# Performance work log

Measured on AMD Instinct MI355X. Metric: run time of the kernel, lower is better.

Reference implementation:

```python
import jax, jax.numpy as jnp
import numpy as np

N = 100_000      # nodes
E = 1_600_000    # edges (before self-loops)
IN = 128         # in_channels
HID = 32         # hidden_channels
HEADS = 2        # attention heads
OUT = 64         # out_channels
NEG_SLOPE = 0.2  # PyG GATConv leaky-relu slope


def setup_inputs() -> dict:
    key = jax.random.key(0)
    ks = jax.random.split(key, 16)
    HC = HID * HEADS

    def glorot(k, shape, fan_in):
        return jax.random.normal(k, shape, jnp.float32) / np.sqrt(fan_in)

    return {
        "x": jax.random.normal(ks[0], (N, IN), jnp.float32),
        "edge_index": jax.random.randint(ks[1], (2, E), 0, N, jnp.int64),
        # layer 1: IN -> HID per head, concat
        "W1": glorot(ks[2], (IN, HC), IN),
        "as1": glorot(ks[3], (HEADS, HID), HID),
        "ad1": glorot(ks[4], (HEADS, HID), HID),
        "b1": jnp.zeros((HC,), jnp.float32),
        # layer 2: HC -> HID per head, concat
        "W2": glorot(ks[5], (HC, HC), HC),
        "as2": glorot(ks[6], (HEADS, HID), HID),
        "ad2": glorot(ks[7], (HEADS, HID), HID),
        "b2": jnp.zeros((HC,), jnp.float32),
        # layer 3: HC -> OUT, 1 head, no concat
        "W3": glorot(ks[8], (HC, OUT), HC),
        "as3": glorot(ks[9], (1, OUT), OUT),
        "ad3": glorot(ks[10], (1, OUT), OUT),
        "b3": jnp.zeros((OUT,), jnp.float32),
    }


def gat_conv(x, src, dst, W, a_src, a_dst, b, heads, out_ch, concat, n):
    # per-head linear transform: [n, heads, out_ch]
    h = (x @ W).reshape(n, heads, out_ch)
    # per-node attention logits: [n, heads]
    al_src = jnp.einsum('nhc,hc->nh', h, a_src)
    al_dst = jnp.einsum('nhc,hc->nh', h, a_dst)
    # raw edge scores with leaky relu: [e, heads]
    e = al_src[src] + al_dst[dst]
    e = jnp.where(e >= 0, e, NEG_SLOPE * e)
    # segment softmax over incoming edges of each dst node
    m = jax.ops.segment_max(e, dst, num_segments=n)          # [n, heads]
    ee = jnp.exp(e - m[dst])
    denom = jax.ops.segment_sum(ee, dst, num_segments=n)     # [n, heads]
    alpha = ee / denom[dst]
    # weighted scatter-add of source features
    out = jax.ops.segment_sum(h[src] * alpha[..., None], dst, num_segments=n)
    if concat:
        out = out.reshape(n, heads * out_ch)
    else:
        out = out.mean(axis=1)
    return out + b


def reference(x, edge_index, W1, as1, ad1, b1, W2, as2, ad2, b2, W3, as3, ad3, b3):
    # PyG GATConv adds self-loops by default
    loop = jnp.arange(N, dtype=edge_index.dtype)
    src = jnp.concatenate([edge_index[0], loop])
    dst = jnp.concatenate([edge_index[1], loop])

    h = gat_conv(x, src, dst, W1, as1, ad1, b1, HEADS, HID, True, N)
    h = jax.nn.relu(h)
    h = gat_conv(h, src, dst, W2, as2, ad2, b2, HEADS, HID, True, N)
    h = jax.nn.relu(h)
    out = gat_conv(h, src, dst, W3, as3, ad3, b3, 1, OUT, False, N)
    return out
```

## Files before the change

### kernel.cpp

```cpp
#include <hip/hip_runtime.h>
#include <hip/hip_fp16.h>

#define IN_CH   128
#define HC      64
#define NEG_SLOPE 0.2f

#define BSH   9
#define NPB   512
#define EPB   8192
#define DBIN  64

typedef __attribute__((ext_vector_type(8))) _Float16 f16x8;
typedef __attribute__((ext_vector_type(4))) float    f32x4;

__global__ __launch_bounds__(256) void scan1_k(const int* __restrict__ deg, int* __restrict__ tmp,
                                               int* __restrict__ bsum, int n) {
    __shared__ int s[256];
    int tid = threadIdx.x;
    int i = blockIdx.x * 256 + tid;
    int v = (i < n) ? deg[i] : 0;
    s[tid] = v; __syncthreads();
    for (int o = 1; o < 256; o <<= 1) {
        int t = (tid >= o) ? s[tid - o] : 0;
        __syncthreads();
        s[tid] += t;
        __syncthreads();
    }
    if (i < n) tmp[i] = s[tid] - v;
    if (tid == 255) bsum[blockIdx.x] = s[255];
}

__global__ __launch_bounds__(512) void scan2_k(int* __restrict__ bsum, int nb) {
    __shared__ int s[512];
    int tid = threadIdx.x;
    int v = (tid < nb) ? bsum[tid] : 0;
    s[tid] = v; __syncthreads();
    for (int o = 1; o < 512; o <<= 1) {
        int t = (tid >= o) ? s[tid - o] : 0;
        __syncthreads();
        s[tid] += t;
        __syncthreads();
    }
    if (tid < nb) bsum[tid] = s[tid] - v;
}

__global__ __launch_bounds__(256) void combine_k(const int* __restrict__ tmp, const int* __restrict__ bsum,
                                                 int* __restrict__ base, int n) {
    int i = blockIdx.x * 256 + threadIdx.x;
    if (i < n) base[i] = tmp[i] + bsum[blockIdx.x];
}

__global__ __launch_bounds__(256) void csortA1_k(const int* __restrict__ ei, int* __restrict__ countsT,
                                                 int E, int nbuck, int neb) {
    __shared__ int cnt[256];
    cnt[threadIdx.x] = 0;
    __syncthreads();
    int base = blockIdx.x * EPB;
#pragma unroll
    for (int k = 0; k < EPB / 256; k++) {
        int i = base + k * 256 + threadIdx.x;
        if (i < E) atomicAdd(&cnt[ei[E + i] >> BSH], 1);
    }
    __syncthreads();
    if (threadIdx.x < nbuck) countsT[threadIdx.x * neb + blockIdx.x] = cnt[threadIdx.x];
}

__global__ __launch_bounds__(256) void csortA3_k(const int* __restrict__ ei, const int* __restrict__ baseT,
                                                 unsigned* __restrict__ pairs, int E, int nbuck, int neb) {
    __shared__ int cur[256];
    if (threadIdx.x < nbuck) cur[threadIdx.x] = baseT[threadIdx.x * neb + blockIdx.x];
    __syncthreads();
    int base = blockIdx.x * EPB;
#pragma unroll
    for (int k = 0; k < EPB / 256; k++) {
        int i = base + k * 256 + threadIdx.x;
        if (i < E) {
            int d = ei[E + i];
            int s = ei[i];
            int p = atomicAdd(&cur[d >> BSH], 1);
            pairs[p] = ((unsigned)(d & (NPB - 1)) << 17) | (unsigned)s;
        }
    }
}

__global__ __launch_bounds__(256) void csortB2_k(const unsigned* __restrict__ pairs, const int* __restrict__ baseT,
                                                 int* __restrict__ off, int* __restrict__ csr,
                                                 int N, int E, int nbuck, int neb) {
    __shared__ int cnt[NPB];
    __shared__ int cur[NPB];
    __shared__ int ps[256];
    int b = blockIdx.x;
    int tid = threadIdx.x;
    int rs = baseT[b * neb];
    int re = (b + 1 < nbuck) ? baseT[(b + 1) * neb] : E;

    cnt[tid] = 0; cnt[tid + 256] = 0;
    __syncthreads();
    for (int j = rs + tid; j < re; j += 256)
        atomicAdd(&cnt[pairs[j] >> 17], 1);
    __syncthreads();

    int c0 = cnt[2 * tid], c1 = cnt[2 * tid + 1];
    int pair = c0 + c1;
    ps[tid] = pair;
    __syncthreads();
    for (int o = 1; o < 256; o <<= 1) {
        int t = (tid >= o) ? ps[tid - o] : 0;
        __syncthreads();
        ps[tid] += t;
        __syncthreads();
    }
    int base0 = rs + ps[tid] - pair;
    int n0 = b * NPB + 2 * tid;
    cur[2 * tid] = base0;
    cur[2 * tid + 1] = base0 + c0;
    if (n0 < N)     off[n0] = base0;
    if (n0 + 1 < N) off[n0 + 1] = base0 + c0;
    if (b == nbuck - 1 && tid == 0) off[N] = E;
    if (b == nbuck - 1 && tid < 64) csr[E + tid] = 0;
    __syncthreads();

    for (int j = rs + tid; j < re; j += 256) {
        unsigned v = pairs[j];
        int p = atomicAdd(&cur[v >> 17], 1);
        csr[p] = (int)(v & 0x1FFFF);
    }
}

__global__ __launch_bounds__(256) void dhist_k(const int* __restrict__ off, int* __restrict__ countsD,
                                               int N, int nb) {
    __shared__ int cnt[DBIN];
    if (threadIdx.x < DBIN) cnt[threadIdx.x] = 0;
    __syncthreads();
    int i = blockIdx.x * 256 + threadIdx.x;
    if (i < N) {
        int d = min(off[i + 1] - off[i], DBIN - 1);
        atomicAdd(&cnt[d], 1);
    }
    __syncthreads();
    if (threadIdx.x < DBIN) countsD[threadIdx.x * nb + blockIdx.x] = cnt[threadIdx.x];
}

__global__ __launch_bounds__(256) void drank_k(const int* __restrict__ off, const int* __restrict__ baseD,
                                               int* __restrict__ perm, int N, int nb) {
    __shared__ int cur[DBIN];
    if (threadIdx.x < DBIN) cur[threadIdx.x] = baseD[threadIdx.x * nb + blockIdx.x];
    __syncthreads();
    int i = blockIdx.x * 256 + threadIdx.x;
    if (i < N) {
        int d = min(off[i + 1] - off[i], DBIN - 1);
        int p = atomicAdd(&cur[d], 1);
        perm[p] = i;
    }
}

__global__ __launch_bounds__(256) void wpack_k(const float* __restrict__ W, _Float16* __restrict__ P, int total) {
    int o = blockIdx.x * 256 + threadIdx.x;
    if (o >= total) return;
    int j = o & 7, l = (o >> 3) & 63, t = (o >> 9) & 3, s = o >> 11;
    int row = s * 32 + ((l >> 4) << 3) + j;
    int col = (t << 4) + (l & 15);
    P[o] = (_Float16)W[row * 64 + col];
}

template<int K, int HEADS>
__global__ __launch_bounds__(256) void gemm_mfma_k(const float* __restrict__ X, const _Float16* __restrict__ P,
                                                   const float* __restrict__ a_s, const float* __restrict__ a_d,
                                                   __half* __restrict__ H, float* __restrict__ ALS,
                                                   float* __restrict__ ALD, int n) {
    __shared__ _Float16 lh[4][16 * 72];
    int tid = threadIdx.x;
    int wv = tid >> 6, lane = tid & 63;
    int wid = blockIdx.x * 4 + wv;
    int rowbase = wid << 4;
    if (rowbase >= n) return;
    int q = lane >> 4, cl = lane & 15;

    f16x8 b[K / 32][4];
    const f16x8* Pv = (const f16x8*)P;
#pragma unroll
    for (int s = 0; s < K / 32; s++)
#pragma unroll
        for (int t = 0; t < 4; t++)
            b[s][t] = Pv[(s * 4 + t) * 64 + lane];

    f32x4 c[4];
#pragma unroll
    for (int t = 0; t < 4; t++) c[t] = (f32x4){0.f, 0.f, 0.f, 0.f};

    const float* xrow = X + (size_t)(rowbase + cl) * K + q * 8;
#pragma unroll
    for (int s = 0; s < K / 32; s++) {
        float4 x0 = *(const float4*)(xrow + s * 32);
        float4 x1 = *(const float4*)(xrow + s * 32 + 4);
        f16x8 a;
        a[0] = (_Float16)x0.x; a[1] = (_Float16)x0.y; a[2] = (_Float16)x0.z; a[3] = (_Float16)x0.w;
        a[4] = (_Float16)x1.x; a[5] = (_Float16)x1.y; a[6] = (_Float16)x1.z; a[7] = (_Float16)x1.w;
#pragma unroll
        for (int t = 0; t < 4; t++)
            c[t] = __builtin_amdgcn_mfma_f32_16x16x32_f16(a, b[s][t], c[t], 0, 0, 0);
    }

    if (HEADS == 2) {
        float as0 = a_s[cl], as1 = a_s[16 + cl], as2 = a_s[32 + cl], as3 = a_s[48 + cl];
        float ad0 = a_d[cl], ad1 = a_d[16 + cl], ad2 = a_d[32 + cl], ad3 = a_d[48 + cl];
#pragma unroll
        for (int reg = 0; reg < 4; reg++) {
            float s0 = c[0][reg] * as0 + c[1][reg] * as1;
            float d0 = c[0][reg] * ad0 + c[1][reg] * ad1;
            float s1 = c[2][reg] * as2 + c[3][reg] * as3;
            float d1 = c[2][reg] * ad2 + c[3][reg] * ad3;
#pragma unroll
            for (int m = 1; m <= 8; m <<= 1) {
                s0 += __shfl_xor(s0, m, 64);
                d0 += __shfl_xor(d0, m, 64);
                s1 += __shfl_xor(s1, m, 64);
                d1 += __shfl_xor(d1, m, 64);
            }
            if (cl == 0) {
                int row = rowbase + q * 4 + reg;
                ALS[row * 2]     = s0;
                ALS[row * 2 + 1] = s1;
                ALD[row * 2]     = d0;
                ALD[row * 2 + 1] = d1;
            }
        }
    } else {
        float as0 = a_s[cl], as1 = a_s[16 + cl], as2 = a_s[32 + cl], as3 = a_s[48 + cl];
        float ad0 = a_d[cl], ad1 = a_d[16 + cl], ad2 = a_d[32 + cl], ad3 = a_d[48 + cl];
#pragma unroll
        for (int reg = 0; reg < 4; reg++) {
            float s0 = c[0][reg] * as0 + c[1][reg] * as1 + c[2][reg] * as2 + c[3][reg] * as3;
            float d0 = c[0][reg] * ad0 + c[1][reg] * ad1 + c[2][reg] * ad2 + c[3][reg] * ad3;
#pragma unroll
            for (int m = 1; m <= 8; m <<= 1) {
                s0 += __shfl_xor(s0, m, 64);
                d0 += __shfl_xor(d0, m, 64);
            }
            if (cl == 0) {
                int row = rowbase + q * 4 + reg;
                ALS[row] = s0;
                ALD[row] = d0;
            }
        }
    }

    _Float16* L = lh[wv];
#pragma unroll
    for (int t = 0; t < 4; t++)
#pragma unroll
        for (int reg = 0; reg < 4; reg++)
            L[(q * 4 + reg) * 72 + t * 16 + cl] = (_Float16)c[t][reg];
    __builtin_amdgcn_s_waitcnt(0);
    int rr = lane >> 2, seg = lane & 3;
    uint4 v0 = *(const uint4*)((const char*)L + rr * 144 + seg * 32);
    uint4 v1 = *(const uint4*)((const char*)L + rr * 144 + seg * 32 + 16);
    char* hb = (char*)(H + (size_t)rowbase * 64);
    *(uint4*)(hb + rr * 128 + seg * 32)      = v0;
    *(uint4*)(hb + rr * 128 + seg * 32 + 16) = v1;
}

template<int HEADS, int RELU>
__global__ __launch_bounds__(256) void aggregate_k(const __half* __restrict__ H, const float* __restrict__ ALS,
                                                   const float* __restrict__ ALD, const int* __restrict__ off,
                                                   const int* __restrict__ csr, const int* __restrict__ perm,
                                                   const float* __restrict__ bias, float* __restrict__ OUT, int n) {
    int lane = threadIdx.x & 63;
    int wv   = threadIdx.x >> 6;
    int c4   = lane & 15;
    int idx  = blockIdx.x * 16 + wv * 4 + (lane >> 4);
    bool alive = idx < n;
    int dst = perm[alive ? idx : 0];
    int head = (HEADS == 2) ? (c4 >> 3) : 0;

    int b0 = off[dst];
    int len = alive ? (off[dst + 1] - b0) : 0;
    float ald = ALD[dst * HEADS + head];

    float e = ALS[dst * HEADS + head] + ald;
    e = fmaxf(e, NEG_SLOPE * e);
    float ee = alive ? __expf(e) : 0.f;
    float den = ee;
    const uint2* Hq = (const uint2*)H;
    uint2 hv = Hq[dst * 16 + c4];
    float2 hl = __half22float2(*(const __half2*)&hv.x);
    float2 hh = __half22float2(*(const __half2*)&hv.y);
    float a0 = ee * hl.x, a1 = ee * hl.y, a2 = ee * hh.x, a3 = ee * hh.y;

    int lmax = max(len, __shfl_xor(len, 16, 64));
    lmax = max(lmax, __shfl_xor(lmax, 32, 64));

    int j = 0;
    for (; j + 7 < lmax; j += 8) {
        int i0 = b0 + j;
        int s[8];
#pragma unroll
        for (int k = 0; k < 8; k++) s[k] = csr[i0 + k];
        float al[8];
#pragma unroll
        for (int k = 0; k < 8; k++) al[k] = ALS[s[k] * HEADS + head];
        uint2 h[8];
#pragma unroll
        for (int k = 0; k < 8; k++) h[k] = Hq[s[k] * 16 + c4];
#pragma unroll
        for (int k = 0; k < 8; k++) {
            float ek = al[k] + ald;
            ek = fmaxf(ek, NEG_SLOPE * ek);
            float wk = (j + k < len) ? __expf(ek) : 0.f;
            float2 l2 = __half22float2(*(const __half2*)&h[k].x);
            float2 h2 = __half22float2(*(const __half2*)&h[k].y);
            den += wk;
            a0 += wk * l2.x; a1 += wk * l2.y;
            a2 += wk * h2.x; a3 += wk * h2.y;
        }
    }
    for (; j < lmax; j++) {
        int s0 = csr[b0 + j];
        float alv = ALS[s0 * HEADS + head];
        uint2 h0 = Hq[s0 * 16 + c4];
        float e0 = alv + ald;
        e0 = fmaxf(e0, NEG_SLOPE * e0);
        float w0 = (j < len) ? __expf(e0) : 0.f;
        float2 l2 = __half22float2(*(const __half2*)&h0.x);
        float2 h2 = __half22float2(*(const __half2*)&h0.y);
        den += w0;
        a0 += w0 * l2.x; a1 += w0 * l2.y;
        a2 += w0 * h2.x; a3 += w0 * h2.y;
    }

    if (alive) {
        float4 bi = ((const float4*)bias)[c4];
        float rd = 1.f / den;
        float o0 = a0 * rd + bi.x;
        float o1 = a1 * rd + bi.y;
        float o2 = a2 * rd + bi.z;
        float o3 = a3 * rd + bi.w;
        if (RELU) {
            o0 = fmaxf(o0, 0.f); o1 = fmaxf(o1, 0.f);
            o2 = fmaxf(o2, 0.f); o3 = fmaxf(o3, 0.f);
        }
        ((float4*)OUT)[dst * 16 + c4] = make_float4(o0, o1, o2, o3);
    }
}

extern "C" void kernel_launch(void* const* d_in, const int* in_sizes, int n_in,
                              void* d_out, int out_size, void* d_ws, size_t ws_size,
                              hipStream_t stream) {
    const float* x   = (const float*)d_in[0];
    const int*   ei  = (const int*)  d_in[1];
    const float* W1  = (const float*)d_in[2];
    const float* as1 = (const float*)d_in[3];
    const float* ad1 = (const float*)d_in[4];
    const float* b1  = (const float*)d_in[5];
    const float* W2  = (const float*)d_in[6];
    const float* as2 = (const float*)d_in[7];
    const float* ad2 = (const float*)d_in[8];
    const float* b2  = (const float*)d_in[9];
    const float* W3  = (const float*)d_in[10];
    const float* as3 = (const float*)d_in[11];
    const float* ad3 = (const float*)d_in[12];
    const float* b3  = (const float*)d_in[13];

    const int N = in_sizes[0] / IN_CH;
    const int E = in_sizes[1] / 2;
    const int NBUCK = (N + NPB - 1) >> BSH;
    const int NEB   = (E + EPB - 1) / EPB;
    const int NT    = NBUCK * NEB;
    const int NB    = (N + 255) / 256;
    const int ND    = DBIN * NB;

    char* p = (char*)d_ws;
    auto carve = [&](size_t bytes) {
        char* r = p;
        p += (bytes + 255) & ~(size_t)255;
        return r;
    };
    __half*    hbuf    = (__half*)   carve((size_t)N * HC * 2);
    float*     obuf    = (float*)    carve((size_t)N * HC * 4);
    float*     als     = (float*)    carve((size_t)N * 2 * 4);
    float*     ald     = (float*)    carve((size_t)N * 2 * 4);
    int*       off     = (int*)      carve((size_t)(N + 1) * 4);
    int*       tmp     = (int*)      carve((size_t)NT * 4);
    int*       bsum    = (int*)      carve((size_t)((NT + 255) / 256 + 1) * 4);
    int*       csr     = (int*)      carve((size_t)(E + 64) * 4);
    unsigned*  pairs   = (unsigned*) carve((size_t)E * 4);
    int*       countsT = (int*)      carve((size_t)NT * 4);
    int*       baseT   = (int*)      carve((size_t)NT * 4);
    int*       countsD = (int*)      carve((size_t)ND * 4);
    int*       baseD   = (int*)      carve((size_t)ND * 4);
    int*       perm    = (int*)      carve((size_t)N * 4);
    _Float16*  wp1     = (_Float16*) carve((size_t)IN_CH * 64 * 2);
    _Float16*  wp2     = (_Float16*) carve((size_t)64 * 64 * 2);
    _Float16*  wp3     = (_Float16*) carve((size_t)64 * 64 * 2);

    const int NTB = (NT + 255) / 256;
    const int NDB = (ND + 255) / 256;
    const int NW4 = (N + 15) / 16;
    const int NBM = (N / 16 + 3) / 4;

    wpack_k<<<(IN_CH * 64) / 256, 256, 0, stream>>>(W1, wp1, IN_CH * 64);
    wpack_k<<<(64 * 64) / 256, 256, 0, stream>>>(W2, wp2, 64 * 64);
    wpack_k<<<(64 * 64) / 256, 256, 0, stream>>>(W3, wp3, 64 * 64);

    csortA1_k<<<NEB, 256, 0, stream>>>(ei, countsT, E, NBUCK, NEB);
    scan1_k  <<<NTB, 256, 0, stream>>>(countsT, tmp, bsum, NT);
    scan2_k  <<<1, 512, 0, stream>>>(bsum, NTB);
    combine_k<<<NTB, 256, 0, stream>>>(tmp, bsum, baseT, NT);
    csortA3_k<<<NEB, 256, 0, stream>>>(ei, baseT, pairs, E, NBUCK, NEB);
    csortB2_k<<<NBUCK, 256, 0, stream>>>(pairs, baseT, off, csr, N, E, NBUCK, NEB);

    dhist_k  <<<NB, 256, 0, stream>>>(off, countsD, N, NB);
    scan1_k  <<<NDB, 256, 0, stream>>>(countsD, tmp, bsum, ND);
    scan2_k  <<<1, 512, 0, stream>>>(bsum, NDB);
    combine_k<<<NDB, 256, 0, stream>>>(tmp, bsum, baseD, ND);
    drank_k  <<<NB, 256, 0, stream>>>(off, baseD, perm, N, NB);

    gemm_mfma_k<128, 2><<<NBM, 256, 0, stream>>>(x, wp1, as1, ad1, hbuf, als, ald, N);
    aggregate_k<2, 1>  <<<NW4, 256, 0, stream>>>(hbuf, als, ald, off, csr, perm, b1, obuf, N);

    gemm_mfma_k<64, 2><<<NBM, 256, 0, stream>>>(obuf, wp2, as2, ad2, hbuf, als, ald, N);
    aggregate_k<2, 1> <<<NW4, 256, 0, stream>>>(hbuf, als, ald, off, csr, perm, b2, obuf, N);

    gemm_mfma_k<64, 1><<<NBM, 256, 0, stream>>>(obuf, wp3, as3, ad3, hbuf, als, ald, N);
    aggregate_k<1, 0> <<<NW4, 256, 0, stream>>>(hbuf, als, ald, off, csr, perm, b3, (float*)d_out, N);
}
```

Before: 334.8 us.

## Store intermediate activations in fp16 and widen per-lane aggregation to 8 channels

Intermediate layer outputs are now written as fp16 and read directly by the next GEMM, which halves activation write and read traffic and drops the fp32-to-fp16 conversion in the GEMM. The aggregation kernel now gives each lane 8 channels via 16-byte gathers, so one wave covers 8 destination nodes instead of 4 and issues fewer, wider loads per neighbor. This raises register use per lane and widens the max-degree reduction across more nodes per wave, which could increase divergence padding. It also adds fp16 rounding of hidden activations.

Measured after the change: 333.7 us. Within noise of the previous version (-0.3%).

```diff
diff --git a/kernel.cpp b/kernel.cpp
--- a/kernel.cpp
+++ b/kernel.cpp
@@ -163,8 +163,8 @@
     P[o] = (_Float16)W[row * 64 + col];
 }
 
-template<int K, int HEADS>
-__global__ __launch_bounds__(256) void gemm_mfma_k(const float* __restrict__ X, const _Float16* __restrict__ P,
+template<int K, int HEADS, bool F16IN>
+__global__ __launch_bounds__(256) void gemm_mfma_k(const void* __restrict__ Xv, const _Float16* __restrict__ P,
                                                    const float* __restrict__ a_s, const float* __restrict__ a_d,
                                                    __half* __restrict__ H, float* __restrict__ ALS,
                                                    float* __restrict__ ALD, int n) {
@@ -188,14 +188,19 @@
 #pragma unroll
     for (int t = 0; t < 4; t++) c[t] = (f32x4){0.f, 0.f, 0.f, 0.f};
 
-    const float* xrow = X + (size_t)(rowbase + cl) * K + q * 8;
 #pragma unroll
     for (int s = 0; s < K / 32; s++) {
-        float4 x0 = *(const float4*)(xrow + s * 32);
-        float4 x1 = *(const float4*)(xrow + s * 32 + 4);
         f16x8 a;
-        a[0] = (_Float16)x0.x; a[1] = (_Float16)x0.y; a[2] = (_Float16)x0.z; a[3] = (_Float16)x0.w;
-        a[4] = (_Float16)x1.x; a[5] = (_Float16)x1.y; a[6] = (_Float16)x1.z; a[7] = (_Float16)x1.w;
+        if (F16IN) {
+            const _Float16* xrow = (const _Float16*)Xv + (size_t)(rowbase + cl) * K + q * 8;
+            a = *(const f16x8*)(xrow + s * 32);
+        } else {
+            const float* xrow = (const float*)Xv + (size_t)(rowbase + cl) * K + q * 8;
+            float4 x0 = *(const float4*)(xrow + s * 32);
+            float4 x1 = *(const float4*)(xrow + s * 32 + 4);
+            a[0] = (_Float16)x0.x; a[1] = (_Float16)x0.y; a[2] = (_Float16)x0.z; a[3] = (_Float16)x0.w;
+            a[4] = (_Float16)x1.x; a[5] = (_Float16)x1.y; a[6] = (_Float16)x1.z; a[7] = (_Float16)x1.w;
+        }
 #pragma unroll
         for (int t = 0; t < 4; t++)
             c[t] = __builtin_amdgcn_mfma_f32_16x16x32_f16(a, b[s][t], c[t], 0, 0, 0);
@@ -260,18 +265,18 @@
     *(uint4*)(hb + rr * 128 + seg * 32 + 16) = v1;
 }
 
-template<int HEADS, int RELU>
+template<int HEADS, int RELU, bool OUTF16>
 __global__ __launch_bounds__(256) void aggregate_k(const __half* __restrict__ H, const float* __restrict__ ALS,
                                                    const float* __restrict__ ALD, const int* __restrict__ off,
                                                    const int* __restrict__ csr, const int* __restrict__ perm,
-                                                   const float* __restrict__ bias, float* __restrict__ OUT, int n) {
+                                                   const float* __restrict__ bias, void* __restrict__ OUT, int n) {
     int lane = threadIdx.x & 63;
     int wv   = threadIdx.x >> 6;
-    int c4   = lane & 15;
-    int idx  = blockIdx.x * 16 + wv * 4 + (lane >> 4);
+    int c8   = lane & 7;
+    int idx  = blockIdx.x * 32 + wv * 8 + (lane >> 3);
     bool alive = idx < n;
     int dst = perm[alive ? idx : 0];
-    int head = (HEADS == 2) ? (c4 >> 3) : 0;
+    int head = (HEADS == 2) ? (c8 >> 2) : 0;
 
     int b0 = off[dst];
     int len = alive ? (off[dst + 1] - b0) : 0;
@@ -281,13 +286,20 @@
     e = fmaxf(e, NEG_SLOPE * e);
     float ee = alive ? __expf(e) : 0.f;
     float den = ee;
-    const uint2* Hq = (const uint2*)H;
-    uint2 hv = Hq[dst * 16 + c4];
-    float2 hl = __half22float2(*(const __half2*)&hv.x);
-    float2 hh = __half22float2(*(const __half2*)&hv.y);
-    float a0 = ee * hl.x, a1 = ee * hl.y, a2 = ee * hh.x, a3 = ee * hh.y;
-
-    int lmax = max(len, __shfl_xor(len, 16, 64));
+    const uint4* Ho = (const uint4*)H;
+    uint4 hv = Ho[dst * 8 + c8];
+    float acc[8];
+    {
+        float2 p0 = __half22float2(*(const __half2*)&hv.x);
+        float2 p1 = __half22float2(*(const __half2*)&hv.y);
+        float2 p2 = __half22float2(*(const __half2*)&hv.z);
+        float2 p3 = __half22float2(*(const __half2*)&hv.w);
+        acc[0] = ee * p0.x; acc[1] = ee * p0.y; acc[2] = ee * p1.x; acc[3] = ee * p1.y;
+        acc[4] = ee * p2.x; acc[5] = ee * p2.y; acc[6] = ee * p3.x; acc[7] = ee * p3.y;
+    }
+
+    int lmax = max(len, __shfl_xor(len, 8, 64));
+    lmax = max(lmax, __shfl_xor(lmax, 16, 64));
     lmax = max(lmax, __shfl_xor(lmax, 32, 64));
 
     int j = 0;
@@ -299,47 +311,65 @@
         float al[8];
 #pragma unroll
         for (int k = 0; k < 8; k++) al[k] = ALS[s[k] * HEADS + head];
-        uint2 h[8];
-#pragma unroll
-        for (int k = 0; k < 8; k++) h[k] = Hq[s[k] * 16 + c4];
+        uint4 h[8];
+#pragma unroll
+        for (int k = 0; k < 8; k++) h[k] = Ho[s[k] * 8 + c8];
 #pragma unroll
         for (int k = 0; k < 8; k++) {
             float ek = al[k] + ald;
             ek = fmaxf(ek, NEG_SLOPE * ek);
             float wk = (j + k < len) ? __expf(ek) : 0.f;
-            float2 l2 = __half22float2(*(const __half2*)&h[k].x);
-            float2 h2 = __half22float2(*(const __half2*)&h[k].y);
             den += wk;
-            a0 += wk * l2.x; a1 += wk * l2.y;
-            a2 += wk * h2.x; a3 += wk * h2.y;
+            float2 p0 = __half22float2(*(const __half2*)&h[k].x);
+            float2 p1 = __half22float2(*(const __half2*)&h[k].y);
+            float2 p2 = __half22float2(*(const __half2*)&h[k].z);
+            float2 p3 = __half22float2(*(const __half2*)&h[k].w);
+            acc[0] += wk * p0.x; acc[1] += wk * p0.y; acc[2] += wk * p1.x; acc[3] += wk * p1.y;
+            acc[4] += wk * p2.x; acc[5] += wk * p2.y; acc[6] += wk * p3.x; acc[7] += wk * p3.y;
         }
     }
     for (; j < lmax; j++) {
         int s0 = csr[b0 + j];
         float alv = ALS[s0 * HEADS + head];
-        uint2 h0 = Hq[s0 * 16 + c4];
+        uint4 h0 = Ho[s0 * 8 + c8];
         float e0 = alv + ald;
         e0 = fmaxf(e0, NEG_SLOPE * e0);
         float w0 = (j < len) ? __expf(e0) : 0.f;
-        float2 l2 = __half22float2(*(const __half2*)&h0.x);
-        float2 h2 = __half22float2(*(const __half2*)&h0.y);
         den += w0;
-        a0 += w0 * l2.x; a1 += w0 * l2.y;
-        a2 += w0 * h2.x; a3 += w0 * h2.y;
+        float2 p0 = __half22float2(*(const __half2*)&h0.x);
+        float2 p1 = __half22float2(*(const __half2*)&h0.y);
+        float2 p2 = __half22float2(*(const __half2*)&h0.z);
+        float2 p3 = __half22float2(*(const __half2*)&h0.w);
+        acc[0] += w0 * p0.x; acc[1] += w0 * p0.y; acc[2] += w0 * p1.x; acc[3] += w0 * p1.y;
+        acc[4] += w0 * p2.x; acc[5] += w0 * p2.y; acc[6] += w0 * p3.x; acc[7] += w0 * p3.y;
     }
 
     if (alive) {
-        float4 bi = ((const float4*)bias)[c4];
+        float4 b0v = ((const float4*)bias)[2 * c8];
+        float4 b1v = ((const float4*)bias)[2 * c8 + 1];
         float rd = 1.f / den;
-        float o0 = a0 * rd + bi.x;
-        float o1 = a1 * rd + bi.y;
-        float o2 = a2 * rd + bi.z;
-        float o3 = a3 * rd + bi.w;
+        float o[8];
+        o[0] = acc[0] * rd + b0v.x; o[1] = acc[1] * rd + b0v.y;
+        o[2] = acc[2] * rd + b0v.z; o[3] = acc[3] * rd + b0v.w;
+        o[4] = acc[4] * rd + b1v.x; o[5] = acc[5] * rd + b1v.y;
+        o[6] = acc[6] * rd + b1v.z; o[7] = acc[7] * rd + b1v.w;
         if (RELU) {
-            o0 = fmaxf(o0, 0.f); o1 = fmaxf(o1, 0.f);
-            o2 = fmaxf(o2, 0.f); o3 = fmaxf(o3, 0.f);
-        }
-        ((float4*)OUT)[dst * 16 + c4] = make_float4(o0, o1, o2, o3);
+#pragma unroll
+            for (int k = 0; k < 8; k++) o[k] = fmaxf(o[k], 0.f);
+        }
+        if (OUTF16) {
+            __half2 q0 = __floats2half2_rn(o[0], o[1]);
+            __half2 q1 = __floats2half2_rn(o[2], o[3]);
+            __half2 q2 = __floats2half2_rn(o[4], o[5]);
+            __half2 q3 = __floats2half2_rn(o[6], o[7]);
+            uint4 u;
+            u.x = *(unsigned*)&q0; u.y = *(unsigned*)&q1;
+            u.z = *(unsigned*)&q2; u.w = *(unsigned*)&q3;
+            ((uint4*)OUT)[dst * 8 + c8] = u;
+        } else {
+            ((float4*)OUT)[dst * 16 + 2 * c8]     = make_float4(o[0], o[1], o[2], o[3]);
+            ((float4*)OUT)[dst * 16 + 2 * c8 + 1] = make_float4(o[4], o[5], o[6], o[7]);
+        }
     }
 }
 
@@ -376,7 +406,7 @@
         return r;
     };
     __half*    hbuf    = (__half*)   carve((size_t)N * HC * 2);
-    float*     obuf    = (float*)    carve((size_t)N * HC * 4);
+    __half*    obuf    = (__half*)   carve((size_t)N * HC * 2);
     float*     als     = (float*)    carve((size_t)N * 2 * 4);
     float*     ald     = (float*)    carve((size_t)N * 2 * 4);
     int*       off     = (int*)      carve((size_t)(N + 1) * 4);
@@ -395,7 +425,7 @@
 
     const int NTB = (NT + 255) / 256;
     const int NDB = (ND + 255) / 256;
-    const int NW4 = (N + 15) / 16;
+    const int NW8 = (N + 31) / 32;
     const int NBM = (N / 16 + 3) / 4;
 
     wpack_k<<<(IN_CH * 64) / 256, 256, 0, stream>>>(W1, wp1, IN_CH * 64);
@@ -415,12 +445,12 @@
     combine_k<<<NDB, 256, 0, stream>>>(tmp, bsum, baseD, ND);
     drank_k  <<<NB, 256, 0, stream>>>(off, baseD, perm, N, NB);
 
-    gemm_mfma_k<128, 2><<<NBM, 256, 0, stream>>>(x, wp1, as1, ad1, hbuf, als, ald, N);
-    aggregate_k<2, 1>  <<<NW4, 256, 0, stream>>>(hbuf, als, ald, off, csr, perm, b1, obuf, N);
-
-    gemm_mfma_k<64, 2><<<NBM, 256, 0, stream>>>(obuf, wp2, as2, ad2, hbuf, als, ald, N);
-    aggregate_k<2, 1> <<<NW4, 256, 0, stream>>>(hbuf, als, ald, off, csr, perm, b2, obuf, N);
-
-    gemm_mfma_k<64, 1><<<NBM, 256, 0, stream>>>(obuf, wp3, as3, ad3, hbuf, als, ald, N);
-    aggregate_k<1, 0> <<<NW4, 256, 0, stream>>>(hbuf, als, ald, off, csr, perm, b3, (float*)d_out, N);
-}
+    gemm_mfma_k<128, 2, false><<<NBM, 256, 0, stream>>>(x, wp1, as1, ad1, hbuf, als, ald, N);
+    aggregate_k<2, 1, true>   <<<NW8, 256, 0, stream>>>(hbuf, als, ald, off, csr, perm, b1, obuf, N);
+
+    gemm_mfma_k<64, 2, true><<<NBM, 256, 0, stream>>>(obuf, wp2, as2, ad2, hbuf, als, ald, N);
+    aggregate_k<2, 1, true> <<<NW8, 256, 0, stream>>>(hbuf, als, ald, off, csr, perm, b2, obuf, N);
+
+    gemm_mfma_k<64, 1, true><<<NBM, 256, 0, stream>>>(obuf, wp3, as3, ad3, hbuf, als, ald, N);
+    aggregate_k<1, 0, false><<<NW8, 256, 0, stream>>>(hbuf, als, ald, off, csr, perm, b3, d_out, N);
+}
```
